# Performance work log

Hardware: AMD Instinct MI355X
Metric: run time of the kernel (lower is better)

## Reference

```python
import jax, jax.numpy as jnp
import numpy as np

AUX_COEF = 0.001
Z_COEF = 0.001


def setup_inputs() -> dict:
    key = jax.random.key(0)
    ks = jax.random.split(key, 6)
    B, S, H, E, F = 4, 2048, 1024, 8, 2048
    scale_h = 1.0 / np.sqrt(H)
    scale_f = 1.0 / np.sqrt(F)
    return {
        "hidden_states": jax.random.normal(ks[0], (B, S, H), jnp.float32),
        "router_w": jax.random.normal(ks[1], (E, H), jnp.float32) * scale_h,
        "w1": jax.random.normal(ks[2], (E, H, F), jnp.float32) * scale_h,
        "b1": jax.random.normal(ks[3], (E, F), jnp.float32) * 0.01,
        "w2": jax.random.normal(ks[4], (E, F, H), jnp.float32) * scale_f,
        "b2": jax.random.normal(ks[5], (E, H), jnp.float32) * 0.01,
        "num_experts_per_tok": 2,
    }


def reference(hidden_states, router_w, w1, b1, w2, b2, num_experts_per_tok):
    B, S, H = hidden_states.shape
    E = router_w.shape[0]
    x = hidden_states.reshape(-1, H)  # [T, H]

    # Router
    logits = jnp.einsum('th,eh->te', x, router_w)  # [T, E]
    logp = jax.nn.log_softmax(logits, axis=-1)
    probs = jnp.exp(logp)

    # Top-k routing mask (note: original code does NOT weight by top_k probs)
    _, top_idx = jax.lax.top_k(probs, num_experts_per_tok)  # [T, K]
    mask = jax.nn.one_hot(top_idx, E, dtype=x.dtype).sum(axis=-2)  # [T, E] 0/1

    # Losses: KL(probs || uniform) with torch kl_div(batchmean over dim0=B) + z-loss
    ideal = 1.0 / E
    aux_loss = (ideal * (jnp.log(jnp.float32(ideal)) - logp)).sum() / B * AUX_COEF
    z_loss = jnp.mean(jnp.square(logits)) * Z_COEF
    router_loss = aux_loss + z_loss

    # Dense grouped expert MLP, combined with 0/1 routing mask
    h = jnp.einsum('th,ehf->tef', x, w1) + b1  # [T, E, F]
    h = jax.nn.silu(h)
    y = jnp.einsum('tef,efh->teh', h, w2) + b2  # [T, E, H]
    out = jnp.einsum('teh,te->th', y, mask).reshape(B, S, H)
    return out, router_loss
```

## Files before the change

### kernel.cpp

```cpp
#include <hip/hip_runtime.h>
#include <stdint.h>

#define T_TOK 8192
#define H_DIM 1024
#define E_NUM 8
#define F_DIM 2048
#define BATCH 4
#define AUX_COEF 0.001f
#define Z_COEF 0.001f

#define NBLK_TOK 32

#define GBM 128
#define GBN 128
#define GBK 64
#define MT_CAP 18

typedef __bf16 bf16x8 __attribute__((ext_vector_type(8)));
typedef float f32x4 __attribute__((ext_vector_type(4)));

__device__ __forceinline__ unsigned short f2bf(float f) {
    union { float f; uint32_t u; } v; v.f = f;
    uint32_t u = v.u;
    return (unsigned short)((u + 0x7FFFu + ((u >> 16) & 1u)) >> 16);
}
__device__ __forceinline__ float bf2f(unsigned short u) {
    union { uint32_t u; float f; } v; v.u = ((uint32_t)u) << 16; return v.f;
}

__device__ __forceinline__ void gl_lds16(const void* g, void* l) {
    __builtin_amdgcn_global_load_lds((const __attribute__((address_space(1))) uint32_t*)g,
                                     (__attribute__((address_space(3))) uint32_t*)l, 16, 0, 0);
}

__global__ void transpose_conv_kernel(const float* __restrict__ in, unsigned short* __restrict__ out,
                                      int R, int C) {
    __shared__ float tile[32][33];
    int e = blockIdx.z;
    const float* ine = in + (size_t)e * R * C;
    unsigned short* oute = out + (size_t)e * R * C;
    int tx = threadIdx.x & 31, ty = threadIdx.x >> 5;
    int c0 = blockIdx.x * 32, r0 = blockIdx.y * 32;
#pragma unroll
    for (int i = 0; i < 4; i++) {
        int r = r0 + ty + i * 8;
        tile[ty + i * 8][tx] = ine[(size_t)r * C + c0 + tx];
    }
    __syncthreads();
#pragma unroll
    for (int i = 0; i < 4; i++) {
        int c = c0 + ty + i * 8;
        oute[(size_t)c * R + r0 + tx] = f2bf(tile[tx][ty + i * 8]);
    }
}

__global__ void router_kernel(const float* __restrict__ x, const float* __restrict__ rw,
                              unsigned short* __restrict__ xb,
                              int* __restrict__ top2, float2* __restrict__ loss_part) {
    int wave = threadIdx.x >> 6;
    int lane = threadIdx.x & 63;
    int t = blockIdx.x * 4 + wave;
    const float4* xr = (const float4*)(x + (size_t)t * H_DIM);
    float4 xv[4];
#pragma unroll
    for (int k = 0; k < 4; k++) xv[k] = xr[lane + 64 * k];
    uint2* xo = (uint2*)(xb + (size_t)t * H_DIM);
#pragma unroll
    for (int k = 0; k < 4; k++) {
        uint2 o;
        o.x = (uint32_t)f2bf(xv[k].x) | ((uint32_t)f2bf(xv[k].y) << 16);
        o.y = (uint32_t)f2bf(xv[k].z) | ((uint32_t)f2bf(xv[k].w) << 16);
        xo[lane + 64 * k] = o;
    }
    float acc[E_NUM];
#pragma unroll
    for (int e = 0; e < E_NUM; e++) {
        const float4* rr = (const float4*)(rw + e * H_DIM);
        float s = 0.f;
#pragma unroll
        for (int k = 0; k < 4; k++) {
            float4 r = rr[lane + 64 * k];
            s += xv[k].x * r.x + xv[k].y * r.y + xv[k].z * r.z + xv[k].w * r.w;
        }
        acc[e] = s;
    }
#pragma unroll
    for (int e = 0; e < E_NUM; e++) {
        float v = acc[e];
#pragma unroll
        for (int off = 32; off; off >>= 1) v += __shfl_xor(v, off);
        acc[e] = v;
    }
    __shared__ float red[8];
    if (lane == 0) {
        float mx = acc[0];
#pragma unroll
        for (int e = 1; e < E_NUM; e++) mx = fmaxf(mx, acc[e]);
        float s = 0.f;
#pragma unroll
        for (int e = 0; e < E_NUM; e++) s += expf(acc[e] - mx);
        float lse = mx + logf(s);
        float slogp = 0.f, ssq = 0.f;
#pragma unroll
        for (int e = 0; e < E_NUM; e++) { slogp += acc[e] - lse; ssq += acc[e] * acc[e]; }
        int i1 = 0; float m1 = acc[0];
#pragma unroll
        for (int e = 1; e < E_NUM; e++) if (acc[e] > m1) { m1 = acc[e]; i1 = e; }
        int i2 = -1; float m2 = -1e30f;
#pragma unroll
        for (int e = 0; e < E_NUM; e++) if (e != i1 && acc[e] > m2) { m2 = acc[e]; i2 = e; }
        top2[t] = i1 | (i2 << 8);
        red[wave] = slogp;
        red[4 + wave] = ssq;
    }
    __syncthreads();
    if (threadIdx.x == 0) {
        float2 p;
        p.x = red[0] + red[1] + red[2] + red[3];
        p.y = red[4] + red[5] + red[6] + red[7];
        loss_part[blockIdx.x] = p;
    }
}

__global__ void hist_kernel(const int* __restrict__ top2, int* __restrict__ blockcounts) {
    __shared__ int cnt[E_NUM];
    if (threadIdx.x < E_NUM) cnt[threadIdx.x] = 0;
    __syncthreads();
    int t = blockIdx.x * 256 + threadIdx.x;
    int v = top2[t];
    atomicAdd(&cnt[v & 255], 1);
    atomicAdd(&cnt[v >> 8], 1);
    __syncthreads();
    if (threadIdx.x < E_NUM) blockcounts[blockIdx.x * E_NUM + threadIdx.x] = cnt[threadIdx.x];
}

__global__ void scan_kernel(const int* __restrict__ blockcounts, const float2* __restrict__ loss_part,
                            int* __restrict__ counts, int* __restrict__ basep, int* __restrict__ offs,
                            float* __restrict__ loss_out) {
    __shared__ float redx[4], redy[4];
    int tid = threadIdx.x;
    float sx = 0.f, sy = 0.f;
    for (int i = tid; i < T_TOK / 4; i += 256) {
        float2 p = loss_part[i];
        sx += p.x; sy += p.y;
    }
#pragma unroll
    for (int off = 32; off; off >>= 1) { sx += __shfl_xor(sx, off); sy += __shfl_xor(sy, off); }
    if ((tid & 63) == 0) { redx[tid >> 6] = sx; redy[tid >> 6] = sy; }
    __syncthreads();
    if (tid == 0) {
        float slogp = redx[0] + redx[1] + redx[2] + redx[3];
        float ssq = redy[0] + redy[1] + redy[2] + redy[3];
        float ideal = 1.0f / E_NUM;
        float aux = ideal * ((float)T_TOK * E_NUM * logf(ideal) - slogp) / BATCH * AUX_COEF;
        float z = ssq / ((float)T_TOK * E_NUM) * Z_COEF;
        loss_out[0] = aux + z;
    }
    if (tid < E_NUM) {
        int s = 0;
        for (int b = 0; b < NBLK_TOK; b++) s += blockcounts[b * E_NUM + tid];
        counts[tid] = s;
    }
    __syncthreads();
    if (tid == 0) {
        int s = 0;
        for (int e = 0; e < E_NUM; e++) { basep[e] = s; s += counts[e]; }
    }
    __syncthreads();
    if (tid < E_NUM) {
        int o = basep[tid];
        for (int b = 0; b < NBLK_TOK; b++) { offs[b * E_NUM + tid] = o; o += blockcounts[b * E_NUM + tid]; }
    }
}

__global__ void scatter_kernel(const int* __restrict__ top2, const int* __restrict__ offs,
                               int* __restrict__ rowlist, int* __restrict__ posv) {
    __shared__ int cur[E_NUM];
    if (threadIdx.x < E_NUM) cur[threadIdx.x] = 0;
    __syncthreads();
    int t = blockIdx.x * 256 + threadIdx.x;
    int v = top2[t];
    int e0 = v & 255, e1 = v >> 8;
    int r0 = atomicAdd(&cur[e0], 1);
    int r1 = atomicAdd(&cur[e1], 1);
    int p0 = offs[blockIdx.x * E_NUM + e0] + r0;
    int p1 = offs[blockIdx.x * E_NUM + e1] + r1;
    rowlist[p0] = t;
    rowlist[p1] = t;
    posv[t] = p0 | (p1 << 16);
}

__global__ void combine_kernel(const int* __restrict__ top2, const int* __restrict__ posv,
                               const unsigned short* __restrict__ ybuf, const float* __restrict__ b2,
                               float* __restrict__ out) {
    int t = blockIdx.x;
    int v = top2[t];
    int p = posv[t];
    int e0 = v & 255, e1 = v >> 8;
    int p0 = p & 0xffff, p1 = (p >> 16) & 0xffff;
    int i = threadIdx.x;
    const ushort4* y0 = (const ushort4*)(ybuf + (size_t)p0 * H_DIM);
    const ushort4* y1 = (const ushort4*)(ybuf + (size_t)p1 * H_DIM);
    const float4* q0 = (const float4*)(b2 + (size_t)e0 * H_DIM);
    const float4* q1 = (const float4*)(b2 + (size_t)e1 * H_DIM);
    ushort4 a = y0[i], b = y1[i];
    float4 c0 = q0[i], c1 = q1[i];
    float4 o;
    o.x = bf2f(a.x) + bf2f(b.x) + c0.x + c1.x;
    o.y = bf2f(a.y) + bf2f(b.y) + c0.y + c1.y;
    o.z = bf2f(a.z) + bf2f(b.z) + c0.z + c1.z;
    o.w = bf2f(a.w) + bf2f(b.w) + c0.w + c1.w;
    ((float4*)(out + (size_t)t * H_DIM))[i] = o;
}

template<int KD, int NTILES_N, bool IS_G1>
__global__ __launch_bounds__(256, 2)
void gemm8p(const unsigned short* __restrict__ A,
            const unsigned short* __restrict__ Bt,
            const float* __restrict__ bias_p,
            const int* __restrict__ rowlist,
            const int* __restrict__ basep,
            const int* __restrict__ counts,
            unsigned short* __restrict__ Out)
{
    constexpr int ND = NTILES_N * GBN;
    constexpr int NKT = KD / GBK;
    static_assert(NKT >= 4, "pipeline needs >=4 K-tiles");

    int bid = blockIdx.x;
    int e = bid & 7;
    int q = bid >> 3;
    int nt = q % NTILES_N;
    int mt = q / NTILES_N;
    int n_e = counts[e];
    if (mt * GBM >= n_e) return;
    int base_e = basep[e];

    __shared__ __attribute__((aligned(16))) unsigned char lds[2][32768];

    int tid = threadIdx.x;
    int wv = tid >> 6, lane = tid & 63;

    int srow = tid >> 3;
    int gc = (tid & 7) ^ (srow & 7);
    const unsigned short* aS[4];
    const unsigned short* bS[4];
#pragma unroll
    for (int i = 0; i < 4; i++) {
        int r = srow + i * 32;
        size_t ra;
        if (IS_G1) {
            int rr = min(mt * GBM + r, n_e - 1);
            ra = (size_t)rowlist[base_e + rr];
        } else {
            ra = (size_t)(base_e + min(mt * GBM + r, n_e - 1));
        }
        aS[i] = A + ra * KD + gc * 8;
        bS[i] = Bt + ((size_t)e * ND + nt * GBN + r) * KD + gc * 8;
    }

    auto stageA = [&](int buf, int h, int t) {
        char* d = (char*)lds + buf * 32768 + h * 8192 + wv * 1024;
        gl_lds16(aS[h * 2 + 0] + t * GBK, d);
        gl_lds16(aS[h * 2 + 1] + t * GBK, d + 4096);
    };
    auto stageB = [&](int buf, int h, int t) {
        char* d = (char*)lds + buf * 32768 + 16384 + h * 8192 + wv * 1024;
        gl_lds16(bS[h * 2 + 0] + t * GBK, d);
        gl_lds16(bS[h * 2 + 1] + t * GBK, d + 4096);
    };

    int mlane = lane & 15, quad = lane >> 4;
    int wr = (wv >> 1) * 64;
    int wc = (wv & 1) * 64;
    int xk0 = (quad * 16) ^ ((mlane & 7) << 4);
    int xk1 = (64 + quad * 16) ^ ((mlane & 7) << 4);
    int aRow = (wr + mlane) * 128;
    int bRow = 16384 + (wc + mlane) * 128;

    f32x4 acc[4][4] = {};
    bf16x8 a01[2][2], a23[2][2], b01[2][2], b23[2][2];

    stageA(0, 0, 0); stageA(0, 1, 0); stageB(0, 0, 0); stageB(0, 1, 0);
    stageB(1, 0, 1); stageA(1, 0, 1);
    asm volatile("s_waitcnt vmcnt(4)" ::: "memory");
    __builtin_amdgcn_s_barrier();

    for (int t = 0; t < NKT; ++t) {
        const char* Ab = (const char*)lds + (t & 1) * 32768;
        int nb = (t + 1) & 1;

#pragma unroll
        for (int mi = 0; mi < 2; mi++) {
            a01[mi][0] = *(const bf16x8*)(Ab + aRow + mi * 2048 + xk0);
            a01[mi][1] = *(const bf16x8*)(Ab + aRow + mi * 2048 + xk1);
        }
#pragma unroll
        for (int ni = 0; ni < 2; ni++) {
            b01[ni][0] = *(const bf16x8*)(Ab + bRow + ni * 2048 + xk0);
            b01[ni][1] = *(const bf16x8*)(Ab + bRow + ni * 2048 + xk1);
        }
        if (t + 1 < NKT) stageB(nb, 1, t + 1);
        __builtin_amdgcn_s_barrier();
        asm volatile("s_waitcnt lgkmcnt(0)" ::: "memory");
        __builtin_amdgcn_sched_barrier(0);
        __builtin_amdgcn_s_setprio(1);
#pragma unroll
        for (int ks = 0; ks < 2; ks++)
#pragma unroll
            for (int mi = 0; mi < 2; mi++)
#pragma unroll
                for (int ni = 0; ni < 2; ni++)
                    acc[mi][ni] = __builtin_amdgcn_mfma_f32_16x16x32_bf16(a01[mi][ks], b01[ni][ks], acc[mi][ni], 0, 0, 0);
        __builtin_amdgcn_s_setprio(0);
        __builtin_amdgcn_s_barrier();

#pragma unroll
        for (int ni = 0; ni < 2; ni++) {
            b23[ni][0] = *(const bf16x8*)(Ab + bRow + (ni + 2) * 2048 + xk0);
            b23[ni][1] = *(const bf16x8*)(Ab + bRow + (ni + 2) * 2048 + xk1);
        }
        if (t + 1 < NKT) stageA(nb, 1, t + 1);
        __builtin_amdgcn_s_barrier();
        asm volatile("s_waitcnt lgkmcnt(0)" ::: "memory");
        __builtin_amdgcn_sched_barrier(0);
        __builtin_amdgcn_s_setprio(1);
#pragma unroll
        for (int ks = 0; ks < 2; ks++)
#pragma unroll
            for (int mi = 0; mi < 2; mi++)
#pragma unroll
                for (int ni = 0; ni < 2; ni++)
                    acc[mi][ni + 2] = __builtin_amdgcn_mfma_f32_16x16x32_bf16(a01[mi][ks], b23[ni][ks], acc[mi][ni + 2], 0, 0, 0);
        __builtin_amdgcn_s_setprio(0);
        __builtin_amdgcn_s_barrier();

#pragma unroll
        for (int mi = 0; mi < 2; mi++) {
            a23[mi][0] = *(const bf16x8*)(Ab + aRow + (mi + 2) * 2048 + xk0);
            a23[mi][1] = *(const bf16x8*)(Ab + aRow + (mi + 2) * 2048 + xk1);
        }
        if (t + 2 < NKT) stageB(t & 1, 0, t + 2);
        __builtin_amdgcn_s_barrier();
        asm volatile("s_waitcnt lgkmcnt(0)" ::: "memory");
        __builtin_amdgcn_sched_barrier(0);
        __builtin_amdgcn_s_setprio(1);
#pragma unroll
        for (int ks = 0; ks < 2; ks++)
#pragma unroll
            for (int mi = 0; mi < 2; mi++)
#pragma unroll
                for (int ni = 0; ni < 2; ni++)
                    acc[mi + 2][ni] = __builtin_amdgcn_mfma_f32_16x16x32_bf16(a23[mi][ks], b01[ni][ks], acc[mi + 2][ni], 0, 0, 0);
        __builtin_amdgcn_s_setprio(0);
        __builtin_amdgcn_s_barrier();

        if (t + 2 < NKT) stageA(t & 1, 0, t + 2);
        __builtin_amdgcn_s_barrier();
        __builtin_amdgcn_sched_barrier(0);
        __builtin_amdgcn_s_setprio(1);
#pragma unroll
        for (int ks = 0; ks < 2; ks++)
#pragma unroll
            for (int mi = 0; mi < 2; mi++)
#pragma unroll
                for (int ni = 0; ni < 2; ni++)
                    acc[mi + 2][ni + 2] = __builtin_amdgcn_mfma_f32_16x16x32_bf16(a23[mi][ks], b23[ni][ks], acc[mi + 2][ni + 2], 0, 0, 0);
        __builtin_amdgcn_s_setprio(0);
        if (t + 2 < NKT) {
            asm volatile("s_waitcnt vmcnt(4)" ::: "memory");
        } else {
            asm volatile("s_waitcnt vmcnt(0)" ::: "memory");
        }
        __builtin_amdgcn_s_barrier();
    }

    float bias[4];
#pragma unroll
    for (int ni = 0; ni < 4; ni++) {
        if (IS_G1) bias[ni] = bias_p[(size_t)e * ND + nt * GBN + wc + ni * 16 + mlane];
        else bias[ni] = 0.f;
    }
#pragma unroll
    for (int mi = 0; mi < 4; mi++) {
        int mbase = mt * GBM + wr + mi * 16 + quad * 4;
#pragma unroll
        for (int r = 0; r < 4; r++) {
            int m = mbase + r;
            if (m < n_e) {
                unsigned short* orow = Out + (size_t)(base_e + m) * ND + nt * GBN + wc + mlane;
#pragma unroll
                for (int ni = 0; ni < 4; ni++) {
                    float c = acc[mi][ni][r] + bias[ni];
                    if (IS_G1) c = c / (1.f + __expf(-c));
                    orow[ni * 16] = f2bf(c);
                }
            }
        }
    }
}

extern "C" void kernel_launch(void* const* d_in, const int* in_sizes, int n_in,
                              void* d_out, int out_size, void* d_ws, size_t ws_size,
                              hipStream_t stream) {
    const float* x = (const float*)d_in[0];
    const float* rw = (const float*)d_in[1];
    const float* w1 = (const float*)d_in[2];
    const float* b1 = (const float*)d_in[3];
    const float* w2 = (const float*)d_in[4];
    const float* b2 = (const float*)d_in[5];
    float* out = (float*)d_out;

    char* ws = (char*)d_ws;
    int* counts      = (int*)(ws + 0);
    int* basep       = (int*)(ws + 64);
    int* blockcounts = (int*)(ws + 128);
    int* offs        = (int*)(ws + 2048);
    float2* loss_part = (float2*)(ws + 4096);
    int* top2        = (int*)(ws + 32768);
    int* rowlist     = (int*)(ws + 65536);
    int* posv        = (int*)(ws + 131072);
    unsigned short* xb  = (unsigned short*)(ws + 163840);
    unsigned short* w1t = (unsigned short*)(ws + 163840 + 16777216ULL);
    unsigned short* w2t = (unsigned short*)(ws + 163840 + 16777216ULL + 33554432ULL);
    unsigned short* h1  = (unsigned short*)(ws + 163840 + 16777216ULL + 2ULL * 33554432ULL);
    unsigned short* ybuf = w1t;

    transpose_conv_kernel<<<dim3(64, 32, 8), 256, 0, stream>>>(w1, w1t, H_DIM, F_DIM);
    transpose_conv_kernel<<<dim3(32, 64, 8), 256, 0, stream>>>(w2, w2t, F_DIM, H_DIM);
    router_kernel<<<T_TOK / 4, 256, 0, stream>>>(x, rw, xb, top2, loss_part);
    hist_kernel<<<NBLK_TOK, 256, 0, stream>>>(top2, blockcounts);
    scan_kernel<<<1, 256, 0, stream>>>(blockcounts, loss_part, counts, basep, offs,
                                       out + (size_t)T_TOK * H_DIM);
    scatter_kernel<<<NBLK_TOK, 256, 0, stream>>>(top2, offs, rowlist, posv);
    gemm8p<H_DIM, F_DIM / GBN, true><<<8 * MT_CAP * (F_DIM / GBN), 256, 0, stream>>>(
        xb, w1t, b1, rowlist, basep, counts, h1);
    gemm8p<F_DIM, H_DIM / GBN, false><<<8 * MT_CAP * (H_DIM / GBN), 256, 0, stream>>>(
        h1, w2t, nullptr, rowlist, basep, counts, ybuf);
    combine_kernel<<<T_TOK, 256, 0, stream>>>(top2, posv, ybuf, b2, out);
}
```

Baseline: 397.8 us.

## Restructure grouped GEMM into ping-pong register-prefetched full-tile pipeline

Replaces the four-phase per-K-tile schedule, which had interleaved partial stages and many barriers, with a whole-tile loop. The loop issues the global-to-LDS load for tile t+2 and reads all of tile t+1's fragments from LDS into a second register set. It then runs all 32 MFMAs for tile t on the current register set. The aim is fewer barriers per K-tile and LDS reads overlapped with MFMA work. In exchange it doubles the fragment registers held live, which could cause spills or lower occupancy under launch_bounds(256,2).

```diff
diff --git a/kernel.cpp b/kernel.cpp
--- a/kernel.cpp
+++ b/kernel.cpp
@@ -215,17 +215,17 @@
 
 template<int KD, int NTILES_N, bool IS_G1>
 __global__ __launch_bounds__(256, 2)
-void gemm8p(const unsigned short* __restrict__ A,
-            const unsigned short* __restrict__ Bt,
-            const float* __restrict__ bias_p,
-            const int* __restrict__ rowlist,
-            const int* __restrict__ basep,
-            const int* __restrict__ counts,
-            unsigned short* __restrict__ Out)
+void gemm_pp(const unsigned short* __restrict__ A,
+             const unsigned short* __restrict__ Bt,
+             const float* __restrict__ bias_p,
+             const int* __restrict__ rowlist,
+             const int* __restrict__ basep,
+             const int* __restrict__ counts,
+             unsigned short* __restrict__ Out)
 {
     constexpr int ND = NTILES_N * GBN;
     constexpr int NKT = KD / GBK;
-    static_assert(NKT >= 4, "pipeline needs >=4 K-tiles");
+    static_assert(NKT >= 4 && (NKT & 1) == 0, "pipeline needs even NKT >= 4");
 
     int bid = blockIdx.x;
     int e = bid & 7;
@@ -259,15 +259,12 @@
         bS[i] = Bt + ((size_t)e * ND + nt * GBN + r) * KD + gc * 8;
     }
 
-    auto stageA = [&](int buf, int h, int t) {
-        char* d = (char*)lds + buf * 32768 + h * 8192 + wv * 1024;
-        gl_lds16(aS[h * 2 + 0] + t * GBK, d);
-        gl_lds16(aS[h * 2 + 1] + t * GBK, d + 4096);
-    };
-    auto stageB = [&](int buf, int h, int t) {
-        char* d = (char*)lds + buf * 32768 + 16384 + h * 8192 + wv * 1024;
-        gl_lds16(bS[h * 2 + 0] + t * GBK, d);
-        gl_lds16(bS[h * 2 + 1] + t * GBK, d + 4096);
+    auto stage_full = [&](int t, int buf) {
+        char* d = (char*)lds + buf * 32768 + wv * 1024;
+#pragma unroll
+        for (int i = 0; i < 4; i++) gl_lds16(aS[i] + t * GBK, d + i * 4096);
+#pragma unroll
+        for (int i = 0; i < 4; i++) gl_lds16(bS[i] + t * GBK, d + 16384 + i * 4096);
     };
 
     int mlane = lane & 15, quad = lane >> 4;
@@ -279,101 +276,68 @@
     int bRow = 16384 + (wc + mlane) * 128;
 
     f32x4 acc[4][4] = {};
-    bf16x8 a01[2][2], a23[2][2], b01[2][2], b23[2][2];
-
-    stageA(0, 0, 0); stageA(0, 1, 0); stageB(0, 0, 0); stageB(0, 1, 0);
-    stageB(1, 0, 1); stageA(1, 0, 1);
-    asm volatile("s_waitcnt vmcnt(4)" ::: "memory");
+    bf16x8 fa0[4][2], fb0[4][2], fa1[4][2], fb1[4][2];
+
+#define READ16(FA, FB, BUFI) do {                                                  \
+    const char* _b = (const char*)lds + (BUFI) * 32768;                            \
+    _Pragma("unroll")                                                              \
+    for (int mi = 0; mi < 4; mi++) {                                               \
+        FA[mi][0] = *(const bf16x8*)(_b + aRow + mi * 2048 + xk0);                 \
+        FA[mi][1] = *(const bf16x8*)(_b + aRow + mi * 2048 + xk1);                 \
+    }                                                                              \
+    _Pragma("unroll")                                                              \
+    for (int ni = 0; ni < 4; ni++) {                                               \
+        FB[ni][0] = *(const bf16x8*)(_b + bRow + ni * 2048 + xk0);                 \
+        FB[ni][1] = *(const bf16x8*)(_b + bRow + ni * 2048 + xk1);                 \
+    }                                                                              \
+} while (0)
+
+#define MFMA32(FA, FB) do {                                                        \
+    __builtin_amdgcn_s_setprio(1);                                                 \
+    _Pragma("unroll")                                                              \
+    for (int ks = 0; ks < 2; ks++)                                                 \
+        _Pragma("unroll")                                                          \
+        for (int mi = 0; mi < 4; mi++)                                             \
+            _Pragma("unroll")                                                      \
+            for (int ni = 0; ni < 4; ni++)                                         \
+                acc[mi][ni] = __builtin_amdgcn_mfma_f32_16x16x32_bf16(             \
+                    FA[mi][ks], FB[ni][ks], acc[mi][ni], 0, 0, 0);                 \
+    __builtin_amdgcn_s_setprio(0);                                                 \
+} while (0)
+
+#define TILE_BODY(T, BUFC, CA, CB, NA, NB) do {                                    \
+    __builtin_amdgcn_s_barrier();                       \
+    __builtin_amdgcn_sched_barrier(0);                                             \
+    if ((T) + 2 < NKT) stage_full((T) + 2, (BUFC));                                \
+    if ((T) + 1 < NKT) {                                                           \
+        if ((T) + 2 < NKT) { asm volatile("s_waitcnt vmcnt(8)" ::: "memory"); }    \
+        else               { asm volatile("s_waitcnt vmcnt(0)" ::: "memory"); }    \
+        __builtin_amdgcn_s_barrier();                       \
+        __builtin_amdgcn_sched_barrier(0);                                         \
+        READ16(NA, NB, (BUFC) ^ 1);                     \
+    }                                                                              \
+    MFMA32(CA, CB);                                                                \
+    asm volatile("s_waitcnt lgkmcnt(0)" ::: "memory");         \
+    __builtin_amdgcn_sched_barrier(0);                                             \
+} while (0)
+
+    stage_full(0, 0);
+    stage_full(1, 1);
+    asm volatile("s_waitcnt vmcnt(8)" ::: "memory");
     __builtin_amdgcn_s_barrier();
-
-    for (int t = 0; t < NKT; ++t) {
-        const char* Ab = (const char*)lds + (t & 1) * 32768;
-        int nb = (t + 1) & 1;
-
-#pragma unroll
-        for (int mi = 0; mi < 2; mi++) {
-            a01[mi][0] = *(const bf16x8*)(Ab + aRow + mi * 2048 + xk0);
-            a01[mi][1] = *(const bf16x8*)(Ab + aRow + mi * 2048 + xk1);
-        }
-#pragma unroll
-        for (int ni = 0; ni < 2; ni++) {
-            b01[ni][0] = *(const bf16x8*)(Ab + bRow + ni * 2048 + xk0);
-            b01[ni][1] = *(const bf16x8*)(Ab + bRow + ni * 2048 + xk1);
-        }
-        if (t + 1 < NKT) stageB(nb, 1, t + 1);
-        __builtin_amdgcn_s_barrier();
-        asm volatile("s_waitcnt lgkmcnt(0)" ::: "memory");
-        __builtin_amdgcn_sched_barrier(0);
-        __builtin_amdgcn_s_setprio(1);
-#pragma unroll
-        for (int ks = 0; ks < 2; ks++)
-#pragma unroll
-            for (int mi = 0; mi < 2; mi++)
-#pragma unroll
-                for (int ni = 0; ni < 2; ni++)
-                    acc[mi][ni] = __builtin_amdgcn_mfma_f32_16x16x32_bf16(a01[mi][ks], b01[ni][ks], acc[mi][ni], 0, 0, 0);
-        __builtin_amdgcn_s_setprio(0);
-        __builtin_amdgcn_s_barrier();
-
-#pragma unroll
-        for (int ni = 0; ni < 2; ni++) {
-            b23[ni][0] = *(const bf16x8*)(Ab + bRow + (ni + 2) * 2048 + xk0);
-            b23[ni][1] = *(const bf16x8*)(Ab + bRow + (ni + 2) * 2048 + xk1);
-        }
-        if (t + 1 < NKT) stageA(nb, 1, t + 1);
-        __builtin_amdgcn_s_barrier();
-        asm volatile("s_waitcnt lgkmcnt(0)" ::: "memory");
-        __builtin_amdgcn_sched_barrier(0);
-        __builtin_amdgcn_s_setprio(1);
-#pragma unroll
-        for (int ks = 0; ks < 2; ks++)
-#pragma unroll
-            for (int mi = 0; mi < 2; mi++)
-#pragma unroll
-                for (int ni = 0; ni < 2; ni++)
-                    acc[mi][ni + 2] = __builtin_amdgcn_mfma_f32_16x16x32_bf16(a01[mi][ks], b23[ni][ks], acc[mi][ni + 2], 0, 0, 0);
-        __builtin_amdgcn_s_setprio(0);
-        __builtin_amdgcn_s_barrier();
-
-#pragma unroll
-        for (int mi = 0; mi < 2; mi++) {
-            a23[mi][0] = *(const bf16x8*)(Ab + aRow + (mi + 2) * 2048 + xk0);
-            a23[mi][1] = *(const bf16x8*)(Ab + aRow + (mi + 2) * 2048 + xk1);
-        }
-        if (t + 2 < NKT) stageB(t & 1, 0, t + 2);
-        __builtin_amdgcn_s_barrier();
-        asm volatile("s_waitcnt lgkmcnt(0)" ::: "memory");
-        __builtin_amdgcn_sched_barrier(0);
-        __builtin_amdgcn_s_setprio(1);
-#pragma unroll
-        for (int ks = 0; ks < 2; ks++)
-#pragma unroll
-            for (int mi = 0; mi < 2; mi++)
-#pragma unroll
-                for (int ni = 0; ni < 2; ni++)
-                    acc[mi + 2][ni] = __builtin_amdgcn_mfma_f32_16x16x32_bf16(a23[mi][ks], b01[ni][ks], acc[mi + 2][ni], 0, 0, 0);
-        __builtin_amdgcn_s_setprio(0);
-        __builtin_amdgcn_s_barrier();
-
-        if (t + 2 < NKT) stageA(t & 1, 0, t + 2);
-        __builtin_amdgcn_s_barrier();
-        __builtin_amdgcn_sched_barrier(0);
-        __builtin_amdgcn_s_setprio(1);
-#pragma unroll
-        for (int ks = 0; ks < 2; ks++)
-#pragma unroll
-            for (int mi = 0; mi < 2; mi++)
-#pragma unroll
-                for (int ni = 0; ni < 2; ni++)
-                    acc[mi + 2][ni + 2] = __builtin_amdgcn_mfma_f32_16x16x32_bf16(a23[mi][ks], b23[ni][ks], acc[mi + 2][ni + 2], 0, 0, 0);
-        __builtin_amdgcn_s_setprio(0);
-        if (t + 2 < NKT) {
-            asm volatile("s_waitcnt vmcnt(4)" ::: "memory");
-        } else {
-            asm volatile("s_waitcnt vmcnt(0)" ::: "memory");
-        }
-        __builtin_amdgcn_s_barrier();
-    }
+    __builtin_amdgcn_sched_barrier(0);
+    READ16(fa0, fb0, 0);
+    asm volatile("s_waitcnt lgkmcnt(0)" ::: "memory");
+    __builtin_amdgcn_sched_barrier(0);
+
+    for (int t2 = 0; t2 < NKT; t2 += 2) {
+        TILE_BODY(t2,     0, fa0, fb0, fa1, fb1);
+        TILE_BODY(t2 + 1, 1, fa1, fb1, fa0, fb0);
+    }
+
+#undef TILE_BODY
+#undef MFMA32
+#undef READ16
 
     float bias[4];
 #pragma unroll
@@ -433,9 +397,9 @@
     scan_kernel<<<1, 256, 0, stream>>>(blockcounts, loss_part, counts, basep, offs,
                                        out + (size_t)T_TOK * H_DIM);
     scatter_kernel<<<NBLK_TOK, 256, 0, stream>>>(top2, offs, rowlist, posv);
-    gemm8p<H_DIM, F_DIM / GBN, true><<<8 * MT_CAP * (F_DIM / GBN), 256, 0, stream>>>(
+    gemm_pp<H_DIM, F_DIM / GBN, true><<<8 * MT_CAP * (F_DIM / GBN), 256, 0, stream>>>(
         xb, w1t, b1, rowlist, basep, counts, h1);
-    gemm8p<F_DIM, H_DIM / GBN, false><<<8 * MT_CAP * (H_DIM / GBN), 256, 0, stream>>>(
+    gemm_pp<F_DIM, H_DIM / GBN, false><<<8 * MT_CAP * (H_DIM / GBN), 256, 0, stream>>>(
         h1, w2t, nullptr, rowlist, basep, counts, ybuf);
     combine_kernel<<<T_TOK, 256, 0, stream>>>(top2, posv, ybuf, b2, out);
 }
```

Measured after the change: 601.3 us. +51.1%, slower.
